# Kernel optimization log

Measured on AMD Instinct MI355X. Metric: run time of the kernel, lower is better.

## Reference

```python
import jax, jax.numpy as jnp
import numpy as np

DEPTH = 4
EPS = 1e-5


def _bn(x, g, b):
    # training-mode BatchNorm over (B,H,W) per channel
    m = x.mean(axis=(0, 2, 3), keepdims=True)
    v = x.var(axis=(0, 2, 3), keepdims=True)
    return (x - m) * jax.lax.rsqrt(v + EPS) * g[None, :, None, None] + b[None, :, None, None]


def _conv_bn(x, w, g, b):
    # 1x1 conv (no bias) + BatchNorm
    y = jnp.einsum('bchw,oc->bohw', x, w)
    return _bn(y, g, b)


def _block_max_broadcast(x, gsz):
    # max over each (H/gsz, W/gsz) block of a gsz x gsz grid, broadcast back
    B, C, H, W = x.shape
    xr = x.reshape(B, C, gsz, H // gsz, gsz, W // gsz)
    m = xr.max(axis=(3, 5), keepdims=True)
    return jnp.broadcast_to(m, xr.shape).reshape(B, C, H, W)


def setup_inputs() -> dict:
    key = jax.random.key(0)
    ks = jax.random.split(key, 3)
    B, C, H, W = 4, 128, 256, 256
    x = jax.random.normal(ks[0], (B, C, H, W), dtype=jnp.float32)
    conv_w = jax.random.normal(ks[1], (DEPTH, C, C), dtype=jnp.float32) * 0.05
    conv_g = jnp.ones((DEPTH, C), dtype=jnp.float32)
    conv_b = jnp.zeros((DEPTH, C), dtype=jnp.float32)
    final_w = jax.random.normal(ks[2], (C, (DEPTH + 1) * C), dtype=jnp.float32) * 0.05
    final_g = jnp.ones((C,), dtype=jnp.float32)
    final_b = jnp.zeros((C,), dtype=jnp.float32)
    return {"x": x, "conv_w": conv_w, "conv_g": conv_g, "conv_b": conv_b,
            "final_w": final_w, "final_g": final_g, "final_b": final_b}


def reference(x, conv_w, conv_g, conv_b, final_w, final_g, final_b):
    # p[0]: identity; p[1+d]: block-max over 2^d x 2^d grid broadcast back, then 1x1 conv+BN
    p = [x]
    for d in range(DEPTH):
        pooled = _block_max_broadcast(x, 2 ** d)  # d=0 -> global max broadcast
        p.append(_conv_bn(pooled, conv_w[d], conv_g[d], conv_b[d]))
    out = jnp.concatenate(p, axis=1)  # [B, 5C, H, W]
    return _conv_bn(out, final_w, final_g, final_b)
```

## Files before the change

kernel.cpp:

```cpp
#include <hip/hip_runtime.h>
#include <hip/hip_bf16.h>
#include <math.h>
#include <float.h>

#define B_ 4
#define C_ 128
#define P_ 65536

#define M3_OFF      0
#define M2_OFF      32768
#define M1_OFF      40960
#define M0_OFF      43008
#define YBASE_      43520
#define SCALED_OFF  87040
#define SHIFTD_OFF  87552
#define CONTRIB_OFF 88064
#define S3_OFF      120832
#define SX_OFF      153600
#define G_OFF       154112
#define SCALEF_OFF  219648
#define SHIFTF_OFF  219776

using short8 = __attribute__((ext_vector_type(8))) short;
using f32x4 = __attribute__((ext_vector_type(4))) float;

__device__ __forceinline__ int level_rel(int d) {
    return YBASE_ - 512 * (((1 << (2 * (d + 1))) - 1) / 3);
}

__device__ __forceinline__ unsigned int bfpair(float a, float b) {
    unsigned int ua = __float_as_uint(a), ub = __float_as_uint(b);
    ua = (ua + 0x7fffu + ((ua >> 16) & 1u)) >> 16;
    ub = (ub + 0x7fffu + ((ub >> 16) & 1u)) & 0xffff0000u;
    return ua | ub;
}

__global__ __launch_bounds__(256) void k_blockmax(const float* __restrict__ x,
                                                  float* __restrict__ ws) {
    int bc = blockIdx.x;
    const float* xp = x + (size_t)bc * P_;
    int t = threadIdx.x, lane = t & 63, wv = t >> 6;
    __shared__ float redm[32], reds[32];
    __shared__ float bm[64], bs[64];
    __shared__ float lv[24];
    for (int br = 0; br < 8; ++br) {
        float m = -FLT_MAX, s = 0.f;
#pragma unroll
        for (int it = 0; it < 8; ++it) {
            int h = br * 32 + it * 4 + wv;
            float4 v = *(const float4*)(xp + (size_t)h * 256 + lane * 4);
            m = fmaxf(m, fmaxf(fmaxf(v.x, v.y), fmaxf(v.z, v.w)));
            s += ((v.x + v.y) + (v.z + v.w));
        }
        m = fmaxf(m, __shfl_xor(m, 1)); s += __shfl_xor(s, 1);
        m = fmaxf(m, __shfl_xor(m, 2)); s += __shfl_xor(s, 2);
        m = fmaxf(m, __shfl_xor(m, 4)); s += __shfl_xor(s, 4);
        if ((lane & 7) == 0) {
            redm[wv * 8 + (lane >> 3)] = m;
            reds[wv * 8 + (lane >> 3)] = s;
        }
        __syncthreads();
        if (t < 8) {
            float mm = fmaxf(fmaxf(redm[t], redm[8 + t]), fmaxf(redm[16 + t], redm[24 + t]));
            float ss = (reds[t] + reds[8 + t]) + (reds[16 + t] + reds[24 + t]);
            bm[br * 8 + t] = mm;
            bs[br * 8 + t] = ss;
            ws[M3_OFF + (size_t)bc * 64 + br * 8 + t] = mm;
            ws[S3_OFF + (size_t)bc * 64 + br * 8 + t] = ss;
        }
        __syncthreads();
    }
    if (t < 8) {
        float sx = 0.f;
        for (int r = 0; r < 8; ++r) sx += bs[t * 8 + r];
        reds[t] = sx;
    }
    if (t < 16) {
        int i2 = t >> 2, j2 = t & 3;
        float m = -FLT_MAX;
        for (int a = 0; a < 2; ++a)
            for (int b2 = 0; b2 < 2; ++b2)
                m = fmaxf(m, bm[(2 * i2 + a) * 8 + 2 * j2 + b2]);
        lv[t] = m;
        ws[M2_OFF + (size_t)bc * 16 + t] = m;
    }
    __syncthreads();
    if (t == 0) {
        float sx = 0.f;
        for (int r = 0; r < 8; ++r) sx += reds[r];
        ws[SX_OFF + bc] = sx;
    }
    if (t < 4) {
        int i1 = t >> 1, j1 = t & 1;
        float m = -FLT_MAX;
        for (int a = 0; a < 2; ++a)
            for (int b2 = 0; b2 < 2; ++b2)
                m = fmaxf(m, lv[(2 * i1 + a) * 4 + 2 * j1 + b2]);
        lv[16 + t] = m;
        ws[M1_OFF + (size_t)bc * 4 + t] = m;
    }
    __syncthreads();
    if (t == 0)
        ws[M0_OFF + bc] = fmaxf(fmaxf(lv[16], lv[17]), fmaxf(lv[18], lv[19]));
}

__global__ __launch_bounds__(256) void k_gram(const float* __restrict__ x,
                                              float* __restrict__ gpart) {
    __shared__ uint4 tileq[2048];
    unsigned char* tile = (unsigned char*)tileq;
    int wg = blockIdx.x;
    int b = wg >> 7, rc = wg & 127;
    const float* xb = x + (size_t)b * C_ * P_ + (size_t)rc * 512;
    int t = threadIdx.x, l = t & 63, wv = t >> 6;
    int pq = t & 31, ci = t >> 5;

    f32x4 acc[2][8];
#pragma unroll
    for (int i = 0; i < 2; ++i)
#pragma unroll
        for (int j = 0; j < 8; ++j) acc[i][j] = (f32x4){0.f, 0.f, 0.f, 0.f};

    for (int s = 0; s < 4; ++s) {
#pragma unroll
        for (int k = 0; k < 16; ++k) {
            int c = ci + 8 * k;
            float4 v = *(const float4*)(xb + (size_t)c * P_ + s * 128 + pq * 4);
            unsigned int u0 = bfpair(v.x, v.y), u1 = bfpair(v.z, v.w);
            int wa = (c * 256 + pq * 8) ^ ((c & 7) << 4);
            *(uint2*)(tile + wa) = make_uint2(u0, u1);
        }
        __syncthreads();
#pragma unroll
        for (int ks = 0; ks < 4; ++ks) {
            int col = ks * 64 + (l >> 4) * 16;
            int ra0 = (((2 * wv) * 16 + (l & 15)) * 256 + col) ^ ((l & 7) << 4);
            int ra1 = (((2 * wv + 1) * 16 + (l & 15)) * 256 + col) ^ ((l & 7) << 4);
            short8 a0 = *(const short8*)(tile + ra0);
            short8 a1 = *(const short8*)(tile + ra1);
#pragma unroll
            for (int nt = 0; nt < 8; ++nt) {
                int rb = ((nt * 16 + (l & 15)) * 256 + col) ^ ((l & 7) << 4);
                short8 bb = *(const short8*)(tile + rb);
                acc[0][nt] = __builtin_amdgcn_mfma_f32_16x16x32_bf16(a0, bb, acc[0][nt], 0, 0, 0);
                acc[1][nt] = __builtin_amdgcn_mfma_f32_16x16x32_bf16(a1, bb, acc[1][nt], 0, 0, 0);
            }
        }
        __syncthreads();
    }
    size_t gb = (size_t)wg * 16384;
#pragma unroll
    for (int mt2 = 0; mt2 < 2; ++mt2) {
        int mt = wv * 2 + mt2;
#pragma unroll
        for (int nt = 0; nt < 8; ++nt)
#pragma unroll
            for (int r = 0; r < 4; ++r)
                gpart[gb + (size_t)(mt * 16 + (l >> 4) * 4 + r) * 128 + nt * 16 + (l & 15)] =
                    acc[mt2][nt][r];
    }
}

__global__ __launch_bounds__(256) void k_reduceG(const float* __restrict__ gpart,
                                                 float* __restrict__ ws) {
    int tid = blockIdx.x * 256 + threadIdx.x;
    int b = tid >> 14, inner = tid & 16383;
    const float* p = gpart + (size_t)b * 128 * 16384 + inner;
    float s = 0.f;
    for (int r = 0; r < 128; ++r) s += p[(size_t)r * 16384];
    ws[G_OFF + tid] = s;
}

__global__ __launch_bounds__(256) void k_conv_pool(const float* __restrict__ conv_w,
                                                   float* __restrict__ ws) {
    int bid = blockIdx.x;
    int d = bid >> 4, b = (bid >> 2) & 3, cchunk = bid & 3;
    int NB = 1 << (2 * d);
    int rel = level_rel(d);
    const float* Mb = ws + rel + (size_t)b * 128 * NB;
    float* Yb = ws + YBASE_ + rel + (size_t)b * 128 * NB;
    __shared__ float mlds[8192];
    int t = threadIdx.x;
    int tot = 128 * NB;
    for (int i = t; i < tot; i += 256) mlds[i] = Mb[i];
    __syncthreads();
    if (NB >= 4) {
        int nbq = NB >> 2;
        int nq = 32 * nbq;
        for (int qi = t; qi < nq; qi += 256) {
            int co = cchunk * 32 + (qi >> (2 * d - 2));
            int bq = qi & (nbq - 1);
            const float* wrow = conv_w + ((size_t)d * 128 + co) * 128;
            float a0 = 0.f, a1 = 0.f, a2 = 0.f, a3 = 0.f;
            for (int ci = 0; ci < 128; ++ci) {
                float4 mv = *(const float4*)(&mlds[ci * NB + bq * 4]);
                float wvv = wrow[ci];
                a0 = fmaf(wvv, mv.x, a0);
                a1 = fmaf(wvv, mv.y, a1);
                a2 = fmaf(wvv, mv.z, a2);
                a3 = fmaf(wvv, mv.w, a3);
            }
            float4 r;
            r.x = a0; r.y = a1; r.z = a2; r.w = a3;
            *(float4*)(&Yb[co * NB + bq * 4]) = r;
        }
    } else {
        for (int oi = t; oi < 32; oi += 256) {
            int co = cchunk * 32 + oi;
            const float* wrow = conv_w + (size_t)co * 128;
            float acc = 0.f;
            for (int ci = 0; ci < 128; ++ci) acc = fmaf(mlds[ci], wrow[ci], acc);
            Yb[co] = acc;
        }
    }
}

__global__ __launch_bounds__(256) void k_bnstats_d(const float* __restrict__ conv_g,
                                                   const float* __restrict__ conv_b,
                                                   float* __restrict__ ws) {
    int tid = blockIdx.x * 256 + threadIdx.x;
    if (tid >= 512) return;
    int d = tid >> 7, c = tid & 127;
    int NB = 1 << (2 * d);
    const float* Y = ws + YBASE_ + level_rel(d);
    int n = 4 * NB;
    float s = 0.f;
    for (int b = 0; b < 4; ++b)
        for (int k = 0; k < NB; ++k) s += Y[((size_t)b * 128 + c) * NB + k];
    float mean = s / (float)n;
    float v = 0.f;
    for (int b = 0; b < 4; ++b)
        for (int k = 0; k < NB; ++k) {
            float dd = Y[((size_t)b * 128 + c) * NB + k] - mean;
            v = fmaf(dd, dd, v);
        }
    float var = v / (float)n;
    float sc = conv_g[d * 128 + c] * rsqrtf(var + 1e-5f);
    ws[SCALED_OFF + tid] = sc;
    ws[SHIFTD_OFF + tid] = conv_b[d * 128 + c] - mean * sc;
}

__global__ __launch_bounds__(128) void k_contrib(const float* __restrict__ final_w,
                                                 float* __restrict__ ws) {
    int b = blockIdx.x >> 6, blk3 = blockIdx.x & 63;
    int i3 = blk3 >> 3, j3 = blk3 & 7;
    __shared__ float pn[512];
    int t = threadIdx.x;
    for (int k = t; k < 512; k += 128) {
        int d = k >> 7, c = k & 127;
        int sh = 3 - d;
        int blkd = (i3 >> sh) * (1 << d) + (j3 >> sh);
        int NB = 1 << (2 * d);
        float yv = ws[YBASE_ + level_rel(d) + ((size_t)b * 128 + c) * NB + blkd];
        pn[k] = yv * ws[SCALED_OFF + k] + ws[SHIFTD_OFF + k];
    }
    __syncthreads();
    const float* fw = final_w + (size_t)t * 640 + 128;
    float acc = 0.f;
#pragma unroll 8
    for (int k = 0; k < 512; k += 4) {
        float4 f = *(const float4*)(fw + k);
        acc = fmaf(pn[k], f.x, acc);
        acc = fmaf(pn[k + 1], f.y, acc);
        acc = fmaf(pn[k + 2], f.z, acc);
        acc = fmaf(pn[k + 3], f.w, acc);
    }
    ws[CONTRIB_OFF + ((size_t)b * 128 + t) * 64 + blk3] = acc;
}

__global__ __launch_bounds__(128) void k_stats(const float* __restrict__ final_w,
                                               const float* __restrict__ final_g,
                                               const float* __restrict__ final_b,
                                               float* __restrict__ ws) {
    int o = blockIdx.x, t = threadIdx.x;
    __shared__ __align__(16) float wlds[128];
    __shared__ __align__(16) float cvl[64];
    __shared__ float rbuf[4];
    wlds[t] = final_w[(size_t)o * 640 + t];
    __syncthreads();
    float SSQ = 0.f, SUM = 0.f;
    for (int b = 0; b < 4; ++b) {
        if (t < 64) cvl[t] = ws[CONTRIB_OFF + (size_t)(b * 128 + o) * 64 + t];
        __syncthreads();
        const float* Gb = ws + G_OFF + (size_t)b * 16384 + (size_t)t * 128;
        float a1 = 0.f;
#pragma unroll 8
        for (int k = 0; k < 128; k += 4) {
            float4 g = *(const float4*)(Gb + k);
            float4 w = *(const float4*)(&wlds[k]);
            a1 = fmaf(g.x, w.x, fmaf(g.y, w.y, fmaf(g.z, w.z, fmaf(g.w, w.w, a1))));
        }
        const float* S3p = ws + S3_OFF + (size_t)(b * 128 + t) * 64;
        float a2 = 0.f;
#pragma unroll 8
        for (int k = 0; k < 64; k += 4) {
            float4 sv = *(const float4*)(S3p + k);
            float4 cv = *(const float4*)(&cvl[k]);
            a2 = fmaf(sv.x, cv.x, fmaf(sv.y, cv.y, fmaf(sv.z, cv.z, fmaf(sv.w, cv.w, a2))));
        }
        float r1 = (a1 + 2.f * a2) * wlds[t];
        float r2 = wlds[t] * ws[SX_OFF + b * 128 + t];
        if (t < 64) {
            r1 += 1024.f * cvl[t] * cvl[t];
            r2 += 1024.f * cvl[t];
        }
#pragma unroll
        for (int k = 1; k < 64; k <<= 1) {
            r1 += __shfl_xor(r1, k);
            r2 += __shfl_xor(r2, k);
        }
        if ((t & 63) == 0) {
            rbuf[(t >> 6) * 2] = r1;
            rbuf[(t >> 6) * 2 + 1] = r2;
        }
        __syncthreads();
        SSQ += rbuf[0] + rbuf[2];
        SUM += rbuf[1] + rbuf[3];
        __syncthreads();
    }
    if (t == 0) {
        float mean = SUM / 262144.f;
        float var = SSQ / 262144.f - mean * mean;
        float sc = final_g[o] * rsqrtf(var + 1e-5f);
        ws[SCALEF_OFF + o] = sc;
        ws[SHIFTF_OFF + o] = final_b[o] - mean * sc;
    }
}

__global__ __launch_bounds__(256) void k_out(const float* __restrict__ x,
                                             const float* __restrict__ final_w,
                                             const float* __restrict__ ws,
                                             float* __restrict__ out) {
    __shared__ uint4 wtileq[2048];
    __shared__ float scl[128], shf[128], cvs[512];
    unsigned char* wtile = (unsigned char*)wtileq;
    int wgid = blockIdx.x;
    int b = wgid >> 9, pt = wgid & 511;
    int p0 = pt * 128;
    int t = threadIdx.x, l = t & 63, wv = t >> 6;
#pragma unroll
    for (int it = 0; it < 32; ++it) {
        int pid = it * 256 + t;
        int o = pid >> 6, cp = (pid & 63) * 2;
        float2 f = *(const float2*)(final_w + (size_t)o * 640 + cp);
        unsigned int u = bfpair(f.x, f.y);
        int wa = (o * 256 + cp * 2) ^ ((o & 7) << 4);
        *(unsigned int*)(wtile + wa) = u;
    }
    if (t < 128) {
        scl[t] = ws[SCALEF_OFF + t];
        shf[t] = ws[SHIFTF_OFF + t];
    }
    int i3 = pt >> 6, jb = (pt & 1) * 4;
    for (int q = t; q < 512; q += 256) {
        int o = q >> 2, jj = q & 3;
        cvs[q] = ws[CONTRIB_OFF + (size_t)(b * 128 + o) * 64 + i3 * 8 + jb + jj];
    }
    __syncthreads();

    const float* xb = x + (size_t)b * C_ * P_;
    int pw = p0 + wv * 32;
    f32x4 acc[8][2];
#pragma unroll
    for (int i = 0; i < 8; ++i) {
        acc[i][0] = (f32x4){0.f, 0.f, 0.f, 0.f};
        acc[i][1] = (f32x4){0.f, 0.f, 0.f, 0.f};
    }
#pragma unroll
    for (int ks = 0; ks < 4; ++ks) {
        short8 bf[2];
#pragma unroll
        for (int nt = 0; nt < 2; ++nt) {
            const float* xp = xb + (size_t)(ks * 32 + (l >> 4) * 8) * P_ + (pw + nt * 16 + (l & 15));
            float f0 = xp[0 * P_], f1 = xp[1 * P_], f2 = xp[2 * P_], f3 = xp[3 * P_];
            float f4 = xp[4 * P_], f5 = xp[5 * P_], f6 = xp[6 * P_], f7 = xp[7 * P_];
            union { uint4 u; short8 s; } cvtu;
            cvtu.u = make_uint4(bfpair(f0, f1), bfpair(f2, f3), bfpair(f4, f5), bfpair(f6, f7));
            bf[nt] = cvtu.s;
        }
#pragma unroll
        for (int mt = 0; mt < 8; ++mt) {
            int ra = ((mt * 16 + (l & 15)) * 256 + ks * 64 + (l >> 4) * 16) ^ ((l & 7) << 4);
            short8 af = *(const short8*)(wtile + ra);
            acc[mt][0] = __builtin_amdgcn_mfma_f32_16x16x32_bf16(af, bf[0], acc[mt][0], 0, 0, 0);
            acc[mt][1] = __builtin_amdgcn_mfma_f32_16x16x32_bf16(af, bf[1], acc[mt][1], 0, 0, 0);
        }
    }
#pragma unroll
    for (int mt = 0; mt < 8; ++mt)
#pragma unroll
        for (int nt = 0; nt < 2; ++nt) {
            int p = pw + nt * 16 + (l & 15);
            int jj = ((p & 255) >> 5) & 3;
#pragma unroll
            for (int r = 0; r < 4; ++r) {
                int o = mt * 16 + (l >> 4) * 4 + r;
                float z = acc[mt][nt][r] + cvs[o * 4 + jj];
                out[(size_t)(b * 128 + o) * P_ + p] = fmaf(z, scl[o], shf[o]);
            }
        }
}

extern "C" void kernel_launch(void* const* d_in, const int* in_sizes, int n_in,
                              void* d_out, int out_size, void* d_ws, size_t ws_size,
                              hipStream_t stream) {
    const float* x = (const float*)d_in[0];
    const float* conv_w = (const float*)d_in[1];
    const float* conv_g = (const float*)d_in[2];
    const float* conv_b = (const float*)d_in[3];
    const float* final_w = (const float*)d_in[4];
    const float* final_g = (const float*)d_in[5];
    const float* final_b = (const float*)d_in[6];
    float* out = (float*)d_out;
    float* ws = (float*)d_ws;

    k_blockmax<<<512, 256, 0, stream>>>(x, ws);
    k_gram<<<512, 256, 0, stream>>>(x, out);
    k_reduceG<<<256, 256, 0, stream>>>(out, ws);
    k_conv_pool<<<64, 256, 0, stream>>>(conv_w, ws);
    k_bnstats_d<<<2, 256, 0, stream>>>(conv_g, conv_b, ws);
    k_contrib<<<B_ * 64, 128, 0, stream>>>(final_w, ws);
    k_stats<<<128, 128, 0, stream>>>(final_w, final_g, final_b, ws);
    k_out<<<2048, 256, 0, stream>>>(x, final_w, ws, out);
}
```

Baseline: 204.8 us.

## Fuse block max/sum pooling into the Gram kernel to avoid re-reading x

```diff
diff --git a/kernel.cpp b/kernel.cpp
--- a/kernel.cpp
+++ b/kernel.cpp
@@ -20,6 +20,8 @@
 #define G_OFF       154112
 #define SCALEF_OFF  219648
 #define SHIFTF_OFF  219776
+#define MAXP_OFF    219904
+#define SUMP_OFF    744192
 
 using short8 = __attribute__((ext_vector_type(8))) short;
 using f32x4 = __attribute__((ext_vector_type(4))) float;
@@ -35,77 +37,9 @@
     return ua | ub;
 }
 
-__global__ __launch_bounds__(256) void k_blockmax(const float* __restrict__ x,
-                                                  float* __restrict__ ws) {
-    int bc = blockIdx.x;
-    const float* xp = x + (size_t)bc * P_;
-    int t = threadIdx.x, lane = t & 63, wv = t >> 6;
-    __shared__ float redm[32], reds[32];
-    __shared__ float bm[64], bs[64];
-    __shared__ float lv[24];
-    for (int br = 0; br < 8; ++br) {
-        float m = -FLT_MAX, s = 0.f;
-#pragma unroll
-        for (int it = 0; it < 8; ++it) {
-            int h = br * 32 + it * 4 + wv;
-            float4 v = *(const float4*)(xp + (size_t)h * 256 + lane * 4);
-            m = fmaxf(m, fmaxf(fmaxf(v.x, v.y), fmaxf(v.z, v.w)));
-            s += ((v.x + v.y) + (v.z + v.w));
-        }
-        m = fmaxf(m, __shfl_xor(m, 1)); s += __shfl_xor(s, 1);
-        m = fmaxf(m, __shfl_xor(m, 2)); s += __shfl_xor(s, 2);
-        m = fmaxf(m, __shfl_xor(m, 4)); s += __shfl_xor(s, 4);
-        if ((lane & 7) == 0) {
-            redm[wv * 8 + (lane >> 3)] = m;
-            reds[wv * 8 + (lane >> 3)] = s;
-        }
-        __syncthreads();
-        if (t < 8) {
-            float mm = fmaxf(fmaxf(redm[t], redm[8 + t]), fmaxf(redm[16 + t], redm[24 + t]));
-            float ss = (reds[t] + reds[8 + t]) + (reds[16 + t] + reds[24 + t]);
-            bm[br * 8 + t] = mm;
-            bs[br * 8 + t] = ss;
-            ws[M3_OFF + (size_t)bc * 64 + br * 8 + t] = mm;
-            ws[S3_OFF + (size_t)bc * 64 + br * 8 + t] = ss;
-        }
-        __syncthreads();
-    }
-    if (t < 8) {
-        float sx = 0.f;
-        for (int r = 0; r < 8; ++r) sx += bs[t * 8 + r];
-        reds[t] = sx;
-    }
-    if (t < 16) {
-        int i2 = t >> 2, j2 = t & 3;
-        float m = -FLT_MAX;
-        for (int a = 0; a < 2; ++a)
-            for (int b2 = 0; b2 < 2; ++b2)
-                m = fmaxf(m, bm[(2 * i2 + a) * 8 + 2 * j2 + b2]);
-        lv[t] = m;
-        ws[M2_OFF + (size_t)bc * 16 + t] = m;
-    }
-    __syncthreads();
-    if (t == 0) {
-        float sx = 0.f;
-        for (int r = 0; r < 8; ++r) sx += reds[r];
-        ws[SX_OFF + bc] = sx;
-    }
-    if (t < 4) {
-        int i1 = t >> 1, j1 = t & 1;
-        float m = -FLT_MAX;
-        for (int a = 0; a < 2; ++a)
-            for (int b2 = 0; b2 < 2; ++b2)
-                m = fmaxf(m, lv[(2 * i1 + a) * 4 + 2 * j1 + b2]);
-        lv[16 + t] = m;
-        ws[M1_OFF + (size_t)bc * 4 + t] = m;
-    }
-    __syncthreads();
-    if (t == 0)
-        ws[M0_OFF + bc] = fmaxf(fmaxf(lv[16], lv[17]), fmaxf(lv[18], lv[19]));
-}
-
-__global__ __launch_bounds__(256) void k_gram(const float* __restrict__ x,
-                                              float* __restrict__ gpart) {
+__global__ __launch_bounds__(256) void k_gram_pool(const float* __restrict__ x,
+                                                   float* __restrict__ ws,
+                                                   float* __restrict__ gpart) {
     __shared__ uint4 tileq[2048];
     unsigned char* tile = (unsigned char*)tileq;
     int wg = blockIdx.x;
@@ -119,12 +53,21 @@
     for (int i = 0; i < 2; ++i)
 #pragma unroll
         for (int j = 0; j < 8; ++j) acc[i][j] = (f32x4){0.f, 0.f, 0.f, 0.f};
-
+    float mx[16][2], sm[16][2];
+#pragma unroll
+    for (int k = 0; k < 16; ++k)
+#pragma unroll
+        for (int par = 0; par < 2; ++par) { mx[k][par] = -FLT_MAX; sm[k][par] = 0.f; }
+
+#pragma unroll
     for (int s = 0; s < 4; ++s) {
 #pragma unroll
         for (int k = 0; k < 16; ++k) {
             int c = ci + 8 * k;
             float4 v = *(const float4*)(xb + (size_t)c * P_ + s * 128 + pq * 4);
+            mx[k][s & 1] = fmaxf(mx[k][s & 1],
+                                 fmaxf(fmaxf(v.x, v.y), fmaxf(v.z, v.w)));
+            sm[k][s & 1] += (v.x + v.y) + (v.z + v.w);
             unsigned int u0 = bfpair(v.x, v.y), u1 = bfpair(v.z, v.w);
             int wa = (c * 256 + pq * 8) ^ ((c & 7) << 4);
             *(uint2*)(tile + wa) = make_uint2(u0, u1);
@@ -158,6 +101,21 @@
                 gpart[gb + (size_t)(mt * 16 + (l >> 4) * 4 + r) * 128 + nt * 16 + (l & 15)] =
                     acc[mt2][nt][r];
     }
+#pragma unroll
+    for (int k = 0; k < 16; ++k)
+#pragma unroll
+        for (int par = 0; par < 2; ++par) {
+            float m = mx[k][par], s2 = sm[k][par];
+            m = fmaxf(m, __shfl_xor(m, 1)); s2 += __shfl_xor(s2, 1);
+            m = fmaxf(m, __shfl_xor(m, 2)); s2 += __shfl_xor(s2, 2);
+            m = fmaxf(m, __shfl_xor(m, 4)); s2 += __shfl_xor(s2, 4);
+            if ((pq & 7) == 0) {
+                int c = ci + 8 * k;
+                int j3 = par * 4 + (pq >> 3);
+                ws[MAXP_OFF + (size_t)wg * 1024 + c * 8 + j3] = m;
+                ws[SUMP_OFF + (size_t)wg * 1024 + c * 8 + j3] = s2;
+            }
+        }
 }
 
 __global__ __launch_bounds__(256) void k_reduceG(const float* __restrict__ gpart,
@@ -168,6 +126,54 @@
     float s = 0.f;
     for (int r = 0; r < 128; ++r) s += p[(size_t)r * 16384];
     ws[G_OFF + tid] = s;
+}
+
+__global__ __launch_bounds__(256) void k_reduceMS(float* __restrict__ ws) {
+    int bc = blockIdx.x * 256 + threadIdx.x;
+    if (bc >= 512) return;
+    int b = bc >> 7, c = bc & 127;
+    float sx = 0.f;
+    for (int blk = 0; blk < 64; ++blk) {
+        int i = blk >> 3, j = blk & 7;
+        float mx = -FLT_MAX, sm = 0.f;
+        for (int rr = 0; rr < 16; ++rr) {
+            size_t idx = (size_t)(b * 128 + i * 16 + rr) * 1024 + c * 8 + j;
+            mx = fmaxf(mx, ws[MAXP_OFF + idx]);
+            sm += ws[SUMP_OFF + idx];
+        }
+        ws[M3_OFF + (size_t)bc * 64 + blk] = mx;
+        ws[S3_OFF + (size_t)bc * 64 + blk] = sm;
+        sx += sm;
+    }
+    ws[SX_OFF + bc] = sx;
+    const float* M3 = ws + (size_t)bc * 64;
+    float* M2 = ws + M2_OFF + (size_t)bc * 16;
+    float* M1 = ws + M1_OFF + (size_t)bc * 4;
+    float m2[16];
+#pragma unroll
+    for (int i2 = 0; i2 < 4; ++i2)
+#pragma unroll
+        for (int j2 = 0; j2 < 4; ++j2) {
+            float m = -FLT_MAX;
+            for (int a = 0; a < 2; ++a)
+                for (int b2 = 0; b2 < 2; ++b2)
+                    m = fmaxf(m, M3[(2 * i2 + a) * 8 + (2 * j2 + b2)]);
+            m2[i2 * 4 + j2] = m;
+            M2[i2 * 4 + j2] = m;
+        }
+    float m1[4];
+#pragma unroll
+    for (int i1 = 0; i1 < 2; ++i1)
+#pragma unroll
+        for (int j1 = 0; j1 < 2; ++j1) {
+            float m = -FLT_MAX;
+            for (int a = 0; a < 2; ++a)
+                for (int b2 = 0; b2 < 2; ++b2)
+                    m = fmaxf(m, m2[(2 * i1 + a) * 4 + (2 * j1 + b2)]);
+            m1[i1 * 2 + j1] = m;
+            M1[i1 * 2 + j1] = m;
+        }
+    ws[M0_OFF + bc] = fmaxf(fmaxf(m1[0], m1[1]), fmaxf(m1[2], m1[3]));
 }
 
 __global__ __launch_bounds__(256) void k_conv_pool(const float* __restrict__ conv_w,
@@ -413,9 +419,9 @@
     float* out = (float*)d_out;
     float* ws = (float*)d_ws;
 
-    k_blockmax<<<512, 256, 0, stream>>>(x, ws);
-    k_gram<<<512, 256, 0, stream>>>(x, out);
+    k_gram_pool<<<512, 256, 0, stream>>>(x, ws, out);
     k_reduceG<<<256, 256, 0, stream>>>(out, ws);
+    k_reduceMS<<<2, 256, 0, stream>>>(ws);
     k_conv_pool<<<64, 256, 0, stream>>>(conv_w, ws);
     k_bnstats_d<<<2, 256, 0, stream>>>(conv_g, conv_b, ws);
     k_contrib<<<B_ * 64, 128, 0, stream>>>(final_w, ws);
```

Result: slower. 450.4 us (+119.9%).

## Fuse block-max/sum pooling into the Gram kernel to share one pass over x

Applied to the files above, without the earlier changes.

```diff
diff --git a/kernel.cpp b/kernel.cpp
--- a/kernel.cpp
+++ b/kernel.cpp
@@ -20,6 +20,8 @@
 #define G_OFF       154112
 #define SCALEF_OFF  219648
 #define SHIFTF_OFF  219776
+#define MAXP_OFF    219904
+#define SUMP_OFF    744192
 
 using short8 = __attribute__((ext_vector_type(8))) short;
 using f32x4 = __attribute__((ext_vector_type(4))) float;
@@ -35,45 +37,126 @@
     return ua | ub;
 }
 
-__global__ __launch_bounds__(256) void k_blockmax(const float* __restrict__ x,
-                                                  float* __restrict__ ws) {
+__global__ __launch_bounds__(256) void k_gram_pool(const float* __restrict__ x,
+                                                   float* __restrict__ ws,
+                                                   float* __restrict__ gpart) {
+    __shared__ uint4 tileq[2048];
+    unsigned char* tile = (unsigned char*)tileq;
+    int wg = blockIdx.x;
+    int b = wg >> 7, rc = wg & 127;
+    const float* xb = x + (size_t)b * C_ * P_ + (size_t)rc * 512;
+    int t = threadIdx.x, l = t & 63, wv = t >> 6;
+    int pq = t & 31, ci = t >> 5;
+
+    f32x4 acc[2][8];
+#pragma unroll
+    for (int i = 0; i < 2; ++i)
+#pragma unroll
+        for (int j = 0; j < 8; ++j) acc[i][j] = (f32x4){0.f, 0.f, 0.f, 0.f};
+    float mx[16][2], sm[16][2];
+#pragma unroll
+    for (int k = 0; k < 16; ++k)
+#pragma unroll
+        for (int par = 0; par < 2; ++par) { mx[k][par] = -FLT_MAX; sm[k][par] = 0.f; }
+
+#pragma unroll
+    for (int s = 0; s < 4; ++s) {
+#pragma unroll
+        for (int k = 0; k < 16; ++k) {
+            int c = ci + 8 * k;
+            float4 v = *(const float4*)(xb + (size_t)c * P_ + s * 128 + pq * 4);
+            mx[k][s & 1] = fmaxf(mx[k][s & 1],
+                                 fmaxf(fmaxf(v.x, v.y), fmaxf(v.z, v.w)));
+            sm[k][s & 1] += (v.x + v.y) + (v.z + v.w);
+            unsigned int u0 = bfpair(v.x, v.y), u1 = bfpair(v.z, v.w);
+            int wa = (c * 256 + pq * 8) ^ ((c & 7) << 4);
+            *(uint2*)(tile + wa) = make_uint2(u0, u1);
+        }
+        __syncthreads();
+#pragma unroll
+        for (int ks = 0; ks < 4; ++ks) {
+            int col = ks * 64 + (l >> 4) * 16;
+            int ra0 = (((2 * wv) * 16 + (l & 15)) * 256 + col) ^ ((l & 7) << 4);
+            int ra1 = (((2 * wv + 1) * 16 + (l & 15)) * 256 + col) ^ ((l & 7) << 4);
+            short8 a0 = *(const short8*)(tile + ra0);
+            short8 a1 = *(const short8*)(tile + ra1);
+#pragma unroll
+            for (int nt = 0; nt < 8; ++nt) {
+                int rb = ((nt * 16 + (l & 15)) * 256 + col) ^ ((l & 7) << 4);
+                short8 bb = *(const short8*)(tile + rb);
+                acc[0][nt] = __builtin_amdgcn_mfma_f32_16x16x32_bf16(a0, bb, acc[0][nt], 0, 0, 0);
+                acc[1][nt] = __builtin_amdgcn_mfma_f32_16x16x32_bf16(a1, bb, acc[1][nt], 0, 0, 0);
+            }
+        }
+        __syncthreads();
+    }
+    size_t gb = (size_t)wg * 16384;
+#pragma unroll
+    for (int mt2 = 0; mt2 < 2; ++mt2) {
+        int mt = wv * 2 + mt2;
+#pragma unroll
+        for (int nt = 0; nt < 8; ++nt)
+#pragma unroll
+            for (int r = 0; r < 4; ++r)
+                gpart[gb + (size_t)(mt * 16 + (l >> 4) * 4 + r) * 128 + nt * 16 + (l & 15)] =
+                    acc[mt2][nt][r];
+    }
+    int i3 = rc >> 4, rr = rc & 15;
+#pragma unroll
+    for (int k = 0; k < 16; ++k)
+#pragma unroll
+        for (int par = 0; par < 2; ++par) {
+            float m = mx[k][par], s2 = sm[k][par];
+            m = fmaxf(m, __shfl_xor(m, 1)); s2 += __shfl_xor(s2, 1);
+            m = fmaxf(m, __shfl_xor(m, 2)); s2 += __shfl_xor(s2, 2);
+            m = fmaxf(m, __shfl_xor(m, 4)); s2 += __shfl_xor(s2, 4);
+            if ((pq & 7) == 0) {
+                int c = ci + 8 * k;
+                int j3 = par * 4 + (pq >> 3);
+                size_t idx = ((size_t)(b * 128 + c) * 64 + i3 * 8 + j3) * 16 + rr;
+                ws[MAXP_OFF + idx] = m;
+                ws[SUMP_OFF + idx] = s2;
+            }
+        }
+}
+
+__global__ __launch_bounds__(256) void k_reduceG(const float* __restrict__ gpart,
+                                                 float* __restrict__ ws) {
+    int tid = blockIdx.x * 256 + threadIdx.x;
+    int b = tid >> 14, inner = tid & 16383;
+    const float* p = gpart + (size_t)b * 128 * 16384 + inner;
+    float s = 0.f;
+    for (int r = 0; r < 128; ++r) s += p[(size_t)r * 16384];
+    ws[G_OFF + tid] = s;
+}
+
+__global__ __launch_bounds__(256) void k_reduceMS(float* __restrict__ ws) {
     int bc = blockIdx.x;
-    const float* xp = x + (size_t)bc * P_;
-    int t = threadIdx.x, lane = t & 63, wv = t >> 6;
-    __shared__ float redm[32], reds[32];
+    int t = threadIdx.x;
+    int blk = t >> 2, q = t & 3;
     __shared__ float bm[64], bs[64];
     __shared__ float lv[24];
-    for (int br = 0; br < 8; ++br) {
-        float m = -FLT_MAX, s = 0.f;
-#pragma unroll
-        for (int it = 0; it < 8; ++it) {
-            int h = br * 32 + it * 4 + wv;
-            float4 v = *(const float4*)(xp + (size_t)h * 256 + lane * 4);
-            m = fmaxf(m, fmaxf(fmaxf(v.x, v.y), fmaxf(v.z, v.w)));
-            s += ((v.x + v.y) + (v.z + v.w));
-        }
+    __shared__ float sxr[8];
+    {
+        size_t base = (size_t)bc * 1024 + blk * 16 + q * 4;
+        float4 mv = *(const float4*)(ws + MAXP_OFF + base);
+        float4 sv = *(const float4*)(ws + SUMP_OFF + base);
+        float m = fmaxf(fmaxf(mv.x, mv.y), fmaxf(mv.z, mv.w));
+        float s = (sv.x + sv.y) + (sv.z + sv.w);
         m = fmaxf(m, __shfl_xor(m, 1)); s += __shfl_xor(s, 1);
         m = fmaxf(m, __shfl_xor(m, 2)); s += __shfl_xor(s, 2);
-        m = fmaxf(m, __shfl_xor(m, 4)); s += __shfl_xor(s, 4);
-        if ((lane & 7) == 0) {
-            redm[wv * 8 + (lane >> 3)] = m;
-            reds[wv * 8 + (lane >> 3)] = s;
-        }
-        __syncthreads();
-        if (t < 8) {
-            float mm = fmaxf(fmaxf(redm[t], redm[8 + t]), fmaxf(redm[16 + t], redm[24 + t]));
-            float ss = (reds[t] + reds[8 + t]) + (reds[16 + t] + reds[24 + t]);
-            bm[br * 8 + t] = mm;
-            bs[br * 8 + t] = ss;
-            ws[M3_OFF + (size_t)bc * 64 + br * 8 + t] = mm;
-            ws[S3_OFF + (size_t)bc * 64 + br * 8 + t] = ss;
-        }
-        __syncthreads();
-    }
+        if (q == 0) {
+            bm[blk] = m;
+            bs[blk] = s;
+            ws[M3_OFF + (size_t)bc * 64 + blk] = m;
+            ws[S3_OFF + (size_t)bc * 64 + blk] = s;
+        }
+    }
+    __syncthreads();
     if (t < 8) {
         float sx = 0.f;
         for (int r = 0; r < 8; ++r) sx += bs[t * 8 + r];
-        reds[t] = sx;
+        sxr[t] = sx;
     }
     if (t < 16) {
         int i2 = t >> 2, j2 = t & 3;
@@ -87,7 +170,7 @@
     __syncthreads();
     if (t == 0) {
         float sx = 0.f;
-        for (int r = 0; r < 8; ++r) sx += reds[r];
+        for (int r = 0; r < 8; ++r) sx += sxr[r];
         ws[SX_OFF + bc] = sx;
     }
     if (t < 4) {
@@ -102,72 +185,6 @@
     __syncthreads();
     if (t == 0)
         ws[M0_OFF + bc] = fmaxf(fmaxf(lv[16], lv[17]), fmaxf(lv[18], lv[19]));
-}
-
-__global__ __launch_bounds__(256) void k_gram(const float* __restrict__ x,
-                                              float* __restrict__ gpart) {
-    __shared__ uint4 tileq[2048];
-    unsigned char* tile = (unsigned char*)tileq;
-    int wg = blockIdx.x;
-    int b = wg >> 7, rc = wg & 127;
-    const float* xb = x + (size_t)b * C_ * P_ + (size_t)rc * 512;
-    int t = threadIdx.x, l = t & 63, wv = t >> 6;
-    int pq = t & 31, ci = t >> 5;
-
-    f32x4 acc[2][8];
-#pragma unroll
-    for (int i = 0; i < 2; ++i)
-#pragma unroll
-        for (int j = 0; j < 8; ++j) acc[i][j] = (f32x4){0.f, 0.f, 0.f, 0.f};
-
-    for (int s = 0; s < 4; ++s) {
-#pragma unroll
-        for (int k = 0; k < 16; ++k) {
-            int c = ci + 8 * k;
-            float4 v = *(const float4*)(xb + (size_t)c * P_ + s * 128 + pq * 4);
-            unsigned int u0 = bfpair(v.x, v.y), u1 = bfpair(v.z, v.w);
-            int wa = (c * 256 + pq * 8) ^ ((c & 7) << 4);
-            *(uint2*)(tile + wa) = make_uint2(u0, u1);
-        }
-        __syncthreads();
-#pragma unroll
-        for (int ks = 0; ks < 4; ++ks) {
-            int col = ks * 64 + (l >> 4) * 16;
-            int ra0 = (((2 * wv) * 16 + (l & 15)) * 256 + col) ^ ((l & 7) << 4);
-            int ra1 = (((2 * wv + 1) * 16 + (l & 15)) * 256 + col) ^ ((l & 7) << 4);
-            short8 a0 = *(const short8*)(tile + ra0);
-            short8 a1 = *(const short8*)(tile + ra1);
-#pragma unroll
-            for (int nt = 0; nt < 8; ++nt) {
-                int rb = ((nt * 16 + (l & 15)) * 256 + col) ^ ((l & 7) << 4);
-                short8 bb = *(const short8*)(tile + rb);
-                acc[0][nt] = __builtin_amdgcn_mfma_f32_16x16x32_bf16(a0, bb, acc[0][nt], 0, 0, 0);
-                acc[1][nt] = __builtin_amdgcn_mfma_f32_16x16x32_bf16(a1, bb, acc[1][nt], 0, 0, 0);
-            }
-        }
-        __syncthreads();
-    }
-    size_t gb = (size_t)wg * 16384;
-#pragma unroll
-    for (int mt2 = 0; mt2 < 2; ++mt2) {
-        int mt = wv * 2 + mt2;
-#pragma unroll
-        for (int nt = 0; nt < 8; ++nt)
-#pragma unroll
-            for (int r = 0; r < 4; ++r)
-                gpart[gb + (size_t)(mt * 16 + (l >> 4) * 4 + r) * 128 + nt * 16 + (l & 15)] =
-                    acc[mt2][nt][r];
-    }
-}
-
-__global__ __launch_bounds__(256) void k_reduceG(const float* __restrict__ gpart,
-                                                 float* __restrict__ ws) {
-    int tid = blockIdx.x * 256 + threadIdx.x;
-    int b = tid >> 14, inner = tid & 16383;
-    const float* p = gpart + (size_t)b * 128 * 16384 + inner;
-    float s = 0.f;
-    for (int r = 0; r < 128; ++r) s += p[(size_t)r * 16384];
-    ws[G_OFF + tid] = s;
 }
 
 __global__ __launch_bounds__(256) void k_conv_pool(const float* __restrict__ conv_w,
@@ -413,9 +430,9 @@
     float* out = (float*)d_out;
     float* ws = (float*)d_ws;
 
-    k_blockmax<<<512, 256, 0, stream>>>(x, ws);
-    k_gram<<<512, 256, 0, stream>>>(x, out);
+    k_gram_pool<<<512, 256, 0, stream>>>(x, ws, out);
     k_reduceG<<<256, 256, 0, stream>>>(out, ws);
+    k_reduceMS<<<512, 256, 0, stream>>>(ws);
     k_conv_pool<<<64, 256, 0, stream>>>(conv_w, ws);
     k_bnstats_d<<<2, 256, 0, stream>>>(conv_g, conv_b, ws);
     k_contrib<<<B_ * 64, 128, 0, stream>>>(final_w, ws);
```

Result: slower. 209.3 us (+2.2%).
